# Kernel optimization log

Hardware: AMD Instinct MI355X
Metric: run time of the kernel (lower is better)

Reference implementation:

```python
import jax, jax.numpy as jnp
import numpy as np

M = 16      # mixture_number
D = 128     # visible_dimension
C = 50      # maxcounts + 1 categories per visible dim (uniform)
B = 32768   # batch size


def setup_inputs() -> dict:
    key = jax.random.key(0)
    k1, k2, k3 = jax.random.split(key, 3)
    x = jax.random.randint(k1, (B, D), 0, C, dtype=jnp.int64)  # integer labels
    mixture_weight = jax.random.normal(k2, (M,), dtype=jnp.float32)
    # cate[i][j] in torch is a length-(C) logit vector; uniform C lets us pack [M, D, C]
    cate = jax.random.normal(k3, (M, D, C), dtype=jnp.float32)
    return {"x": x, "mixture_weight": mixture_weight, "cate": cate}


def reference(x, mixture_weight, cate):
    # eval mode: label_smoothing = 0, so CE(logits, y) = -log_softmax(logits)[y]
    logw = jax.nn.log_softmax(mixture_weight)          # [M]
    logp = jax.nn.log_softmax(cate, axis=-1)           # [M, D, C]
    # gather log-prob of each observed category: [M, B, D]
    g = jnp.take_along_axis(logp[:, None, :, :], x[None, :, :, None], axis=3)[..., 0]
    # loss_all = -sum_j CE = sum_j log p; add log mixture weight -> [M, B]
    ll = g.sum(axis=-1) + logw[:, None]
    return jax.nn.logsumexp(ll, axis=0)                # [B]
```

## Files before the change

kernel.cpp:

```cpp
#include <hip/hip_runtime.h>
#include <hip/hip_bf16.h>

#define MM 16
#define DD 128
#define CC 50
#define BB 32768

__global__ __launch_bounds__(256) void prep_kernel(
    const float* __restrict__ cate,
    const float* __restrict__ mw,
    unsigned short* __restrict__ tabw,
    float* __restrict__ logw)
{
    const int wid  = (blockIdx.x * 256 + threadIdx.x) >> 6;
    const int lane = threadIdx.x & 63;
    const int m = wid >> 7;
    const int d = wid & (DD - 1);

    const float* row = cate + (m * DD + d) * CC;
    float v = (lane < CC) ? row[lane] : -1e30f;

    float mx = v;
    #pragma unroll
    for (int off = 32; off; off >>= 1)
        mx = fmaxf(mx, __shfl_xor(mx, off, 64));
    float e = (lane < CC) ? __expf(v - mx) : 0.f;
    #pragma unroll
    for (int off = 32; off; off >>= 1)
        e += __shfl_xor(e, off, 64);
    float lse = mx + __logf(e);

    if (lane < CC) {
        float lp = v - lse;
        unsigned int bits = __float_as_uint(lp);
        bits += 0x7fffu + ((bits >> 16) & 1u);
        tabw[(d * CC + lane) * MM + m] = (unsigned short)(bits >> 16);
    }

    if (wid == 0 && lane < MM) {
        float mw_l = mw[lane];
        float mmx = -1e30f;
        #pragma unroll
        for (int i = 0; i < MM; ++i) mmx = fmaxf(mmx, mw[i]);
        float s = 0.f;
        #pragma unroll
        for (int i = 0; i < MM; ++i) s += __expf(mw[i] - mmx);
        logw[lane] = mw_l - (mmx + __logf(s));
    }
}

__global__ __launch_bounds__(256) void gather_kernel(
    const int* __restrict__ x,
    const unsigned int* __restrict__ tab,
    const float* __restrict__ logw,
    float* __restrict__ out)
{
    const int tid  = threadIdx.x;
    const int l    = tid & 7;
    const int bsub = tid >> 3;
    const int b    = blockIdx.x * 32 + bsub;

    const int4* __restrict__ xrow = (const int4*)(x + b * DD);
    const unsigned int* __restrict__ t = tab + l;

    float accx = 0.f, accy = 0.f;
    #pragma unroll 8
    for (int d4 = 0; d4 < DD / 4; ++d4) {
        int4 xv = xrow[d4];
        int base = d4 * (4 * CC * 8);
        unsigned int u0 = t[base             + xv.x * 8];
        unsigned int u1 = t[base + 1*CC*8    + xv.y * 8];
        unsigned int u2 = t[base + 2*CC*8    + xv.z * 8];
        unsigned int u3 = t[base + 3*CC*8    + xv.w * 8];
        accx += __uint_as_float(u0 << 16) + __uint_as_float(u1 << 16)
              + __uint_as_float(u2 << 16) + __uint_as_float(u3 << 16);
        accy += __uint_as_float(u0 & 0xffff0000u) + __uint_as_float(u1 & 0xffff0000u)
              + __uint_as_float(u2 & 0xffff0000u) + __uint_as_float(u3 & 0xffff0000u);
    }

    float llx = accx + logw[2 * l];
    float lly = accy + logw[2 * l + 1];

    float mx = fmaxf(llx, lly);
    #pragma unroll
    for (int off = 4; off; off >>= 1)
        mx = fmaxf(mx, __shfl_xor(mx, off, 64));
    float e = __expf(llx - mx) + __expf(lly - mx);
    #pragma unroll
    for (int off = 4; off; off >>= 1)
        e += __shfl_xor(e, off, 64);

    if (l == 0) out[b] = mx + __logf(e);
}

extern "C" void kernel_launch(void* const* d_in, const int* in_sizes, int n_in,
                              void* d_out, int out_size, void* d_ws, size_t ws_size,
                              hipStream_t stream) {
    const int*   x    = (const int*)d_in[0];
    const float* mw   = (const float*)d_in[1];
    const float* cate = (const float*)d_in[2];
    float* out = (float*)d_out;

    unsigned short* tabw = (unsigned short*)d_ws;
    float* logw = (float*)((char*)d_ws + (size_t)DD * CC * MM * sizeof(unsigned short));

    prep_kernel<<<(MM * DD) / 4, 256, 0, stream>>>(cate, mw, tabw, logw);

    gather_kernel<<<BB / 32, 256, 0, stream>>>(x, (const unsigned int*)tabw, logw, out);
}
```

Measured before the change: 23.35 us.

## Stage lookup table chunks in LDS and gather with four lanes per row

The gather kernel now copies the bf16 log-prob table into shared memory in 32-dimension chunks, synchronising per chunk, and each batch row is handled by 4 lanes that each accumulate 4 mixtures instead of 8 lanes with 2. Blocks grow to 512 threads covering 128 rows. The intent is to replace scattered global/L2 gathers with LDS gathers and to amortise each x load over more mixtures. The cost is repeated table copies per block, two barriers per chunk, and possible LDS bank conflicts on the data-dependent indices.

```diff
diff --git a/kernel.cpp b/kernel.cpp
--- a/kernel.cpp
+++ b/kernel.cpp
@@ -5,6 +5,7 @@
 #define DD 128
 #define CC 50
 #define BB 32768
+#define DCH 32
 
 __global__ __launch_bounds__(256) void prep_kernel(
     const float* __restrict__ cate,
@@ -49,46 +50,67 @@
     }
 }
 
-__global__ __launch_bounds__(256) void gather_kernel(
+__global__ __launch_bounds__(512) void gather_kernel(
     const int* __restrict__ x,
     const unsigned int* __restrict__ tab,
     const float* __restrict__ logw,
     float* __restrict__ out)
 {
-    const int tid  = threadIdx.x;
-    const int l    = tid & 7;
-    const int bsub = tid >> 3;
-    const int b    = blockIdx.x * 32 + bsub;
+    __shared__ __align__(16) unsigned int lds[DCH * CC * 8];
+
+    const int tid = threadIdx.x;
+    const int l   = tid & 3;
+    const int r   = tid >> 2;
+    const int b   = blockIdx.x * 128 + r;
 
     const int4* __restrict__ xrow = (const int4*)(x + b * DD);
-    const unsigned int* __restrict__ t = tab + l;
 
-    float accx = 0.f, accy = 0.f;
-    #pragma unroll 8
-    for (int d4 = 0; d4 < DD / 4; ++d4) {
-        int4 xv = xrow[d4];
-        int base = d4 * (4 * CC * 8);
-        unsigned int u0 = t[base             + xv.x * 8];
-        unsigned int u1 = t[base + 1*CC*8    + xv.y * 8];
-        unsigned int u2 = t[base + 2*CC*8    + xv.z * 8];
-        unsigned int u3 = t[base + 3*CC*8    + xv.w * 8];
-        accx += __uint_as_float(u0 << 16) + __uint_as_float(u1 << 16)
-              + __uint_as_float(u2 << 16) + __uint_as_float(u3 << 16);
-        accy += __uint_as_float(u0 & 0xffff0000u) + __uint_as_float(u1 & 0xffff0000u)
-              + __uint_as_float(u2 & 0xffff0000u) + __uint_as_float(u3 & 0xffff0000u);
+    float a0 = 0.f, a1 = 0.f, a2 = 0.f, a3 = 0.f;
+
+    #pragma unroll 1
+    for (int ch = 0; ch < DD / DCH; ++ch) {
+        {
+            const float4* __restrict__ src = (const float4*)(tab + ch * (DCH * CC * 8));
+            float4* dst = (float4*)lds;
+            for (int i = tid; i < DCH * CC * 8 / 4; i += 512)
+                dst[i] = src[i];
+        }
+        __syncthreads();
+
+        int4 xv[DCH / 4];
+        #pragma unroll
+        for (int j = 0; j < DCH / 4; ++j)
+            xv[j] = xrow[ch * (DCH / 4) + j];
+
+        #pragma unroll
+        for (int j = 0; j < DCH / 4; ++j) {
+            int cs[4] = { xv[j].x, xv[j].y, xv[j].z, xv[j].w };
+            #pragma unroll
+            for (int k = 0; k < 4; ++k) {
+                int dloc = j * 4 + k;
+                const unsigned int* p = &lds[(dloc * CC + cs[k]) * 8 + 2 * l];
+                unsigned int u0 = p[0];
+                unsigned int u1 = p[1];
+                a0 += __uint_as_float(u0 << 16);
+                a1 += __uint_as_float(u0 & 0xffff0000u);
+                a2 += __uint_as_float(u1 << 16);
+                a3 += __uint_as_float(u1 & 0xffff0000u);
+            }
+        }
+        __syncthreads();
     }
 
-    float llx = accx + logw[2 * l];
-    float lly = accy + logw[2 * l + 1];
+    float l0 = a0 + logw[4 * l + 0];
+    float l1 = a1 + logw[4 * l + 1];
+    float l2 = a2 + logw[4 * l + 2];
+    float l3 = a3 + logw[4 * l + 3];
 
-    float mx = fmaxf(llx, lly);
-    #pragma unroll
-    for (int off = 4; off; off >>= 1)
-        mx = fmaxf(mx, __shfl_xor(mx, off, 64));
-    float e = __expf(llx - mx) + __expf(lly - mx);
-    #pragma unroll
-    for (int off = 4; off; off >>= 1)
-        e += __shfl_xor(e, off, 64);
+    float mx = fmaxf(fmaxf(l0, l1), fmaxf(l2, l3));
+    mx = fmaxf(mx, __shfl_xor(mx, 1, 64));
+    mx = fmaxf(mx, __shfl_xor(mx, 2, 64));
+    float e = __expf(l0 - mx) + __expf(l1 - mx) + __expf(l2 - mx) + __expf(l3 - mx);
+    e += __shfl_xor(e, 1, 64);
+    e += __shfl_xor(e, 2, 64);
 
     if (l == 0) out[b] = mx + __logf(e);
 }
@@ -106,5 +128,5 @@
 
     prep_kernel<<<(MM * DD) / 4, 256, 0, stream>>>(cate, mw, tabw, logw);
 
-    gather_kernel<<<BB / 32, 256, 0, stream>>>(x, (const unsigned int*)tabw, logw, out);
+    gather_kernel<<<BB / 128, 512, 0, stream>>>(x, (const unsigned int*)tabw, logw, out);
 }
```

Measured after the change: 23.93 us. 1.02x slower.

## Split gather over visible dims per thread with 32-byte row loads

Applied to the files above, without the earlier changes.

The gather kernel now gives each of the 8 lanes per batch row a slice of 16 visible dimensions, instead of a pair of mixture components across all dimensions. Each lane loads the full 16-component bf16 row for its category as two uint4 loads and accumulates all 16 mixtures. Partial sums are then combined with shuffle reductions over 16 values. The mixture-weight log-softmax moves from the prep kernel into every gather thread. The goal is fewer, wider and more coalesced table loads and fewer x loads per thread. The cost is more registers, more shuffles and redundant logsumexp work on the weights in every thread.

```diff
diff --git a/kernel.cpp b/kernel.cpp
--- a/kernel.cpp
+++ b/kernel.cpp
@@ -8,9 +8,7 @@
 
 __global__ __launch_bounds__(256) void prep_kernel(
     const float* __restrict__ cate,
-    const float* __restrict__ mw,
-    unsigned short* __restrict__ tabw,
-    float* __restrict__ logw)
+    unsigned short* __restrict__ tabw)
 {
     const int wid  = (blockIdx.x * 256 + threadIdx.x) >> 6;
     const int lane = threadIdx.x & 63;
@@ -31,66 +29,76 @@
     float lse = mx + __logf(e);
 
     if (lane < CC) {
-        float lp = v - lse;
-        unsigned int bits = __float_as_uint(lp);
+        unsigned int bits = __float_as_uint(v - lse);
         bits += 0x7fffu + ((bits >> 16) & 1u);
         tabw[(d * CC + lane) * MM + m] = (unsigned short)(bits >> 16);
-    }
-
-    if (wid == 0 && lane < MM) {
-        float mw_l = mw[lane];
-        float mmx = -1e30f;
-        #pragma unroll
-        for (int i = 0; i < MM; ++i) mmx = fmaxf(mmx, mw[i]);
-        float s = 0.f;
-        #pragma unroll
-        for (int i = 0; i < MM; ++i) s += __expf(mw[i] - mmx);
-        logw[lane] = mw_l - (mmx + __logf(s));
     }
 }
 
 __global__ __launch_bounds__(256) void gather_kernel(
     const int* __restrict__ x,
-    const unsigned int* __restrict__ tab,
-    const float* __restrict__ logw,
+    const uint4* __restrict__ tab,
+    const float* __restrict__ mw,
     float* __restrict__ out)
 {
-    const int tid  = threadIdx.x;
-    const int l    = tid & 7;
-    const int bsub = tid >> 3;
-    const int b    = blockIdx.x * 32 + bsub;
+    const int tid = threadIdx.x;
+    const int h   = tid & 7;
+    const int r   = tid >> 3;
+    const int b   = blockIdx.x * 32 + r;
 
-    const int4* __restrict__ xrow = (const int4*)(x + b * DD);
-    const unsigned int* __restrict__ t = tab + l;
+    float mmx = -1e30f;
+    #pragma unroll
+    for (int k = 0; k < MM; ++k) mmx = fmaxf(mmx, mw[k]);
+    float sw = 0.f;
+    #pragma unroll
+    for (int k = 0; k < MM; ++k) sw += __expf(mw[k] - mmx);
+    float lsew = mmx + __logf(sw);
 
-    float accx = 0.f, accy = 0.f;
-    #pragma unroll 8
-    for (int d4 = 0; d4 < DD / 4; ++d4) {
-        int4 xv = xrow[d4];
-        int base = d4 * (4 * CC * 8);
-        unsigned int u0 = t[base             + xv.x * 8];
-        unsigned int u1 = t[base + 1*CC*8    + xv.y * 8];
-        unsigned int u2 = t[base + 2*CC*8    + xv.z * 8];
-        unsigned int u3 = t[base + 3*CC*8    + xv.w * 8];
-        accx += __uint_as_float(u0 << 16) + __uint_as_float(u1 << 16)
-              + __uint_as_float(u2 << 16) + __uint_as_float(u3 << 16);
-        accy += __uint_as_float(u0 & 0xffff0000u) + __uint_as_float(u1 & 0xffff0000u)
-              + __uint_as_float(u2 & 0xffff0000u) + __uint_as_float(u3 & 0xffff0000u);
+    const int4* __restrict__ xq = (const int4*)(x + b * DD) + h * 4;
+
+    float a[MM];
+    #pragma unroll
+    for (int i = 0; i < MM; ++i) a[i] = 0.f;
+
+    #pragma unroll
+    for (int j = 0; j < 4; ++j) {
+        int4 xv = xq[j];
+        int cs[4] = { xv.x, xv.y, xv.z, xv.w };
+        #pragma unroll
+        for (int k = 0; k < 4; ++k) {
+            int d = h * 16 + j * 4 + k;
+            const uint4* p = tab + (size_t)(d * CC + cs[k]) * 2;
+            uint4 u0 = p[0];
+            uint4 u1 = p[1];
+            unsigned int w[8] = { u0.x, u0.y, u0.z, u0.w,
+                                  u1.x, u1.y, u1.z, u1.w };
+            #pragma unroll
+            for (int q = 0; q < 8; ++q) {
+                a[2 * q]     += __uint_as_float(w[q] << 16);
+                a[2 * q + 1] += __uint_as_float(w[q] & 0xffff0000u);
+            }
+        }
     }
 
-    float llx = accx + logw[2 * l];
-    float lly = accy + logw[2 * l + 1];
+    #pragma unroll
+    for (int off = 1; off < 8; off <<= 1) {
+        #pragma unroll
+        for (int i = 0; i < MM; ++i)
+            a[i] += __shfl_xor(a[i], off, 64);
+    }
 
-    float mx = fmaxf(llx, lly);
+    float ll[MM];
+    float mx = -1e30f;
     #pragma unroll
-    for (int off = 4; off; off >>= 1)
-        mx = fmaxf(mx, __shfl_xor(mx, off, 64));
-    float e = __expf(llx - mx) + __expf(lly - mx);
+    for (int i = 0; i < MM; ++i) {
+        ll[i] = a[i] + mw[i] - lsew;
+        mx = fmaxf(mx, ll[i]);
+    }
+    float e = 0.f;
     #pragma unroll
-    for (int off = 4; off; off >>= 1)
-        e += __shfl_xor(e, off, 64);
+    for (int i = 0; i < MM; ++i) e += __expf(ll[i] - mx);
 
-    if (l == 0) out[b] = mx + __logf(e);
+    if (h == 0) out[b] = mx + __logf(e);
 }
 
 extern "C" void kernel_launch(void* const* d_in, const int* in_sizes, int n_in,
@@ -102,9 +110,8 @@
     float* out = (float*)d_out;
 
     unsigned short* tabw = (unsigned short*)d_ws;
-    float* logw = (float*)((char*)d_ws + (size_t)DD * CC * MM * sizeof(unsigned short));
 
-    prep_kernel<<<(MM * DD) / 4, 256, 0, stream>>>(cate, mw, tabw, logw);
+    prep_kernel<<<(MM * DD) / 4, 256, 0, stream>>>(cate, tabw);
 
-    gather_kernel<<<BB / 32, 256, 0, stream>>>(x, (const unsigned int*)tabw, logw, out);
+    gather_kernel<<<BB / 32, 256, 0, stream>>>(x, (const uint4*)tabw, mw, out);
 }
```

Result: slower. 25.15 us (+7.7%).
